# Performance work log

Hardware: AMD Instinct MI355X
Metric: run time of the kernel (lower is better)

Reference implementation:

```python
import jax, jax.numpy as jnp
import numpy as np

L = 2048  # episode_len
B = 64    # batch
K = 256   # key_size
V = 256   # value_size
H = 8     # num_head


def setup_inputs() -> dict:
    key = jax.random.key(0)
    ks = jax.random.split(key, 9)
    query = jax.random.normal(ks[0], (B, K), dtype=jnp.float32)
    keys = jax.random.normal(ks[1], (L, B, K), dtype=jnp.float32)
    vals = jax.random.normal(ks[2], (L, B, V), dtype=jnp.float32)
    rpe_mod = jax.random.uniform(ks[3], (L, B, 1), dtype=jnp.float32)
    Wq = jax.random.normal(ks[4], (K, H * K), dtype=jnp.float32) * (1.0 / np.sqrt(K))
    bq = jnp.zeros((H * K,), dtype=jnp.float32)
    Wa = jax.random.normal(ks[5], (H * V, V), dtype=jnp.float32) * (1.0 / np.sqrt(H * V))
    ba = jnp.zeros((V,), dtype=jnp.float32)
    # per-sample valid length in [1, L] (nonzero so the softmax is well-defined,
    # matching read()'s early-return guard for empty memories)
    steps = jax.random.randint(ks[6], (B,), 1, L + 1, dtype=jnp.int32)
    return {"query": query, "keys": keys, "vals": vals, "rpe_mod": rpe_mod,
            "Wq": Wq, "bq": bq, "Wa": Wa, "ba": ba, "steps": steps}


def reference(query, keys, vals, rpe_mod, Wq, bq, Wa, ba, steps):
    # query encoder: [B,K] -> [B,H,K]
    q = (query @ Wq + bq).reshape(B, H, K)
    # RPE-modulated keys: [L,B,K]
    mod_keys = keys * rpe_mod
    # scores[l,b,h] = <mod_keys[l,b,:], q[b,h,:]>
    scores = jnp.einsum('lbk,bhk->lbh', mod_keys, q)
    # mask out positions >= steps[b] (equivalent to slicing keys[:step[i], i])
    valid = (jnp.arange(L, dtype=jnp.int32)[:, None] < steps[None, :])  # [L,B]
    scores = jnp.where(valid[:, :, None], scores, -jnp.inf)
    weight = jax.nn.softmax(scores, axis=0)  # softmax over stored steps
    # weighted memory read: [B,H,V]
    read = jnp.einsum('lbh,lbv->bhv', weight, vals)
    # head aggregation: [B, H*V] -> [B, V]
    out = read.reshape(B, H * V) @ Wa + ba
    return out
```

## Files before the change

### kernel.cpp

```cpp
#include <hip/hip_runtime.h>
#include <hip/hip_bf16.h>
#include <cstdint>

#define Ln 2048
#define Bn 64
#define Kd 256
#define Vd 256
#define Hn 8

using u32 = unsigned int;
using u16 = unsigned short;

__device__ __forceinline__ float bflo(u32 u) { return __uint_as_float(u << 16); }
__device__ __forceinline__ float bfhi(u32 u) { return __uint_as_float(u & 0xffff0000u); }
__device__ __forceinline__ float bf1(u16 s) { return __uint_as_float(((u32)s) << 16); }

__device__ __forceinline__ bool sniff_bf16(const void* keys) {
  const u16* q = (const u16*)keys;
  int lane = threadIdx.x & 63;
  u16 u = q[2 * (lane * 127)];
  u32 e = (u >> 7) & 0xff;
  bool sane = (u == 0) || (e >= 100 && e <= 134);
  return __popcll(__ballot(sane)) > 32;
}

__global__ __launch_bounds__(256) void k_prep(const void* keys, const void* query,
                                              const void* Wq, const void* bq,
                                              float* q_ws) {
  const bool bf = sniff_bf16(keys);
  const int t = threadIdx.x;
  const int chunk = blockIdx.x;
  const int b = blockIdx.y;

  __shared__ float ql[256];
  ql[t] = bf ? bf1(((const u16*)query)[b * 256 + t]) : ((const float*)query)[b * 256 + t];
  __syncthreads();

  int c0 = chunk * 512 + 2 * t;
  float a0, a1;
  if (bf) { a0 = bf1(((const u16*)bq)[c0]); a1 = bf1(((const u16*)bq)[c0 + 1]); }
  else    { a0 = ((const float*)bq)[c0];    a1 = ((const float*)bq)[c0 + 1]; }

  if (bf) {
    const u32* w = (const u32*)Wq + chunk * 256 + t;
    for (int k0 = 0; k0 < 256; k0 += 16) {
      u32 wv[16];
#pragma unroll
      for (int j = 0; j < 16; j++) wv[j] = w[(size_t)(k0 + j) * 1024];
#pragma unroll
      for (int j = 0; j < 16; j++) {
        float qk = ql[k0 + j];
        a0 += qk * bflo(wv[j]); a1 += qk * bfhi(wv[j]);
      }
    }
  } else {
    const float2* w = (const float2*)Wq + chunk * 256 + t;
    for (int k0 = 0; k0 < 256; k0 += 16) {
      float2 wv[16];
#pragma unroll
      for (int j = 0; j < 16; j++) wv[j] = w[(size_t)(k0 + j) * 1024];
#pragma unroll
      for (int j = 0; j < 16; j++) {
        float qk = ql[k0 + j];
        a0 += qk * wv[j].x; a1 += qk * wv[j].y;
      }
    }
  }
  q_ws[b * 2048 + c0] = a0;
  q_ws[b * 2048 + c0 + 1] = a1;
}

__global__ __launch_bounds__(256) void k_fused(const void* keys, const void* vals,
                                               const void* rpe, const int* steps,
                                               const float* q_ws, float* O_part,
                                               float2* mz_part) {
  const int b = blockIdx.y, chunk = blockIdx.x;
  const int lstart = chunk * 128;
  const int stepb = steps[b];
  if (lstart >= stepb) return;
  const int lcnt_chunk = min(128, stepb - lstart);
  const bool bf = sniff_bf16(keys);
  const int t = threadIdx.x;
  const float* qb = q_ws + b * 2048;

  union Shm {
    struct { float ks[64 * 132]; float part[4][64][9]; } sc;
    float comb[128 * 20];
  };
  __shared__ Shm u;
  __shared__ __align__(16) float w_lds[128 * 12];
  __shared__ float rpe_lds[128];

  if (t < 128) {
    int l = lstart + t;
    rpe_lds[t] = bf ? bf1(((const u16*)rpe)[l * 64 + b]) : ((const float*)rpe)[l * 64 + b];
  }

  for (int st = 0; st < 2; st++) {
    const int sbase = st * 64;
    if (lstart + sbase >= stepb) continue;
    const int lcnt = min(64, stepb - lstart - sbase);
    const int r = t & 63;
    const int kh = __builtin_amdgcn_readfirstlane(t >> 6);
    float acc[8] = {0, 0, 0, 0, 0, 0, 0, 0};

    for (int khalf = 0; khalf < 2; khalf++) {
      __syncthreads();
      if (bf) {
        int r0 = t >> 4, c = t & 15;
#pragma unroll
        for (int rr = 0; rr < 4; rr++) {
          int row = r0 + rr * 16;
          const uint4* src = (const uint4*)((const u16*)keys +
              ((size_t)(lstart + sbase + row) * 64 + b) * 256 + khalf * 128);
          uint4 uu = src[c];
          float* dst = &u.sc.ks[row * 132 + c * 8];
          float4 lo, hi;
          lo.x = bflo(uu.x); lo.y = bfhi(uu.x); lo.z = bflo(uu.y); lo.w = bfhi(uu.y);
          hi.x = bflo(uu.z); hi.y = bfhi(uu.z); hi.z = bflo(uu.w); hi.w = bfhi(uu.w);
          *(float4*)dst = lo;
          *(float4*)(dst + 4) = hi;
        }
      } else {
        int r0 = t >> 5, c = t & 31;
#pragma unroll
        for (int rr = 0; rr < 8; rr++) {
          int row = r0 + rr * 8;
          const float4* src = (const float4*)((const float*)keys +
              ((size_t)(lstart + sbase + row) * 64 + b) * 256 + khalf * 128);
          *(float4*)&u.sc.ks[row * 132 + c * 4] = src[c];
        }
      }
      __syncthreads();
      if (r < lcnt) {
#pragma unroll
        for (int i = 0; i < 8; i++) {
          float4 kv = *(const float4*)&u.sc.ks[r * 132 + kh * 32 + 4 * i];
          int k0 = khalf * 128 + kh * 32 + 4 * i;
#pragma unroll
          for (int h = 0; h < 8; h++) {
            float4 qv = *(const float4*)&qb[h * 256 + k0];
            acc[h] += kv.x * qv.x + kv.y * qv.y + kv.z * qv.z + kv.w * qv.w;
          }
        }
      }
    }
    __syncthreads();
    if (r < lcnt) {
#pragma unroll
      for (int h = 0; h < 8; h++) u.sc.part[kh][r][h] = acc[h];
    }
    __syncthreads();
#pragma unroll
    for (int i = 0; i < 2; i++) {
      int idx = i * 256 + t;
      int h = idx >> 6, rr = idx & 63;
      if (rr < lcnt) {
        float s = u.sc.part[0][rr][h] + u.sc.part[1][rr][h] +
                  u.sc.part[2][rr][h] + u.sc.part[3][rr][h];
        w_lds[(sbase + rr) * 12 + h] = s * rpe_lds[sbase + rr];
      }
    }
  }
  __syncthreads();

  __shared__ float2 mz_lds[8];
  {
    const int h = t >> 5, j = t & 31;
    float m = -3.0e38f;
#pragma unroll
    for (int i = 0; i < 4; i++) {
      int l = j + 32 * i;
      if (l < lcnt_chunk) m = fmaxf(m, w_lds[l * 12 + h]);
    }
#pragma unroll
    for (int off = 16; off >= 1; off >>= 1) m = fmaxf(m, __shfl_xor(m, off, 32));
    float zs = 0.f;
#pragma unroll
    for (int i = 0; i < 4; i++) {
      int l = j + 32 * i;
      float e = 0.f;
      if (l < lcnt_chunk) e = __expf(w_lds[l * 12 + h] - m);
      w_lds[l * 12 + h] = e;
      zs += e;
    }
#pragma unroll
    for (int off = 16; off >= 1; off >>= 1) zs += __shfl_xor(zs, off, 32);
    if (j == 0) {
      float2 mz; mz.x = m; mz.y = zs;
      mz_lds[h] = mz;
    }
  }
  __syncthreads();
  if (t < 8) mz_part[((size_t)chunk * 64 + b) * 8 + t] = mz_lds[t];

  const int vp = t & 127;
  const int lh = __builtin_amdgcn_readfirstlane(t >> 7);
  float acc[8][2];
#pragma unroll
  for (int h = 0; h < 8; h++) { acc[h][0] = 0.f; acc[h][1] = 0.f; }

  if (bf) {
    const u32* vu = (const u32*)vals + ((size_t)(lstart + lh * 64) * 64 + b) * 128 + vp;
    for (int i0 = 0; i0 < 64; i0 += 8) {
      u32 uu[8];
#pragma unroll
      for (int j = 0; j < 8; j++) uu[j] = vu[(size_t)(i0 + j) * 8192];
#pragma unroll
      for (int j = 0; j < 8; j++) {
        int l = lh * 64 + i0 + j;
        float f0 = bflo(uu[j]), f1 = bfhi(uu[j]);
        float4 w0 = *(const float4*)&w_lds[l * 12];
        float4 w1 = *(const float4*)&w_lds[l * 12 + 4];
        acc[0][0] += w0.x * f0; acc[0][1] += w0.x * f1;
        acc[1][0] += w0.y * f0; acc[1][1] += w0.y * f1;
        acc[2][0] += w0.z * f0; acc[2][1] += w0.z * f1;
        acc[3][0] += w0.w * f0; acc[3][1] += w0.w * f1;
        acc[4][0] += w1.x * f0; acc[4][1] += w1.x * f1;
        acc[5][0] += w1.y * f0; acc[5][1] += w1.y * f1;
        acc[6][0] += w1.z * f0; acc[6][1] += w1.z * f1;
        acc[7][0] += w1.w * f0; acc[7][1] += w1.w * f1;
      }
    }
  } else {
    const float2* vf = (const float2*)vals + ((size_t)(lstart + lh * 64) * 64 + b) * 128 + vp;
    for (int i0 = 0; i0 < 64; i0 += 8) {
      float2 vv[8];
#pragma unroll
      for (int j = 0; j < 8; j++) vv[j] = vf[(size_t)(i0 + j) * 8192];
#pragma unroll
      for (int j = 0; j < 8; j++) {
        int l = lh * 64 + i0 + j;
        float4 w0 = *(const float4*)&w_lds[l * 12];
        float4 w1 = *(const float4*)&w_lds[l * 12 + 4];
        acc[0][0] += w0.x * vv[j].x; acc[0][1] += w0.x * vv[j].y;
        acc[1][0] += w0.y * vv[j].x; acc[1][1] += w0.y * vv[j].y;
        acc[2][0] += w0.z * vv[j].x; acc[2][1] += w0.z * vv[j].y;
        acc[3][0] += w0.w * vv[j].x; acc[3][1] += w0.w * vv[j].y;
        acc[4][0] += w1.x * vv[j].x; acc[4][1] += w1.x * vv[j].y;
        acc[5][0] += w1.y * vv[j].x; acc[5][1] += w1.y * vv[j].y;
        acc[6][0] += w1.z * vv[j].x; acc[6][1] += w1.z * vv[j].y;
        acc[7][0] += w1.w * vv[j].x; acc[7][1] += w1.w * vv[j].y;
      }
    }
  }
  __syncthreads();
  if (lh == 1) {
#pragma unroll
    for (int h = 0; h < 8; h++) {
      u.comb[vp * 20 + 2 * h] = acc[h][0];
      u.comb[vp * 20 + 2 * h + 1] = acc[h][1];
    }
  }
  __syncthreads();
  if (lh == 0) {
    float* op = O_part + ((size_t)chunk * 64 + b) * 2048;
#pragma unroll
    for (int h = 0; h < 8; h++) {
      float2 o;
      o.x = acc[h][0] + u.comb[vp * 20 + 2 * h];
      o.y = acc[h][1] + u.comb[vp * 20 + 2 * h + 1];
      *(float2*)&op[h * 256 + 2 * vp] = o;
    }
  }
}

__global__ __launch_bounds__(256) void k_out1(const void* keys, const void* Wa,
                                              const int* steps, const float* O_part,
                                              const float2* mz_part, float* out_part) {
  const int h = blockIdx.x, b = blockIdx.y;
  const bool bf = sniff_bf16(keys);
  const int t = threadIdx.x;
  const int nlive = (steps[b] + 127) >> 7;

  float2 mzv[16];
#pragma unroll
  for (int c = 0; c < 16; c++)
    mzv[c] = (c < nlive) ? mz_part[((size_t)c * 64 + b) * 8 + h] : make_float2(-3.0e38f, 0.f);
  float M = -3.0e38f;
#pragma unroll
  for (int c = 0; c < 16; c++) M = fmaxf(M, mzv[c].x);
  float sc[16];
  float Z = 0.f;
#pragma unroll
  for (int c = 0; c < 16; c++) {
    sc[c] = __expf(mzv[c].x - M);
    Z += sc[c] * mzv[c].y;
  }
  const float zi = 1.0f / Z;

  __shared__ float rn[256];
  {
    const float* op = O_part + (size_t)b * 2048 + h * 256 + t;
    float ov[16];
#pragma unroll
    for (int c = 0; c < 16; c++) ov[c] = (c < nlive) ? op[(size_t)c * 131072] : 0.f;
    float s = 0.f;
#pragma unroll
    for (int c = 0; c < 16; c++) s += sc[c] * ov[c];
    rn[t] = s * zi;
  }
  __syncthreads();

  float a = 0.f;
  if (bf) {
    const u32* wa = (const u32*)Wa + (size_t)(h * 256) * 128 + (t >> 1);
    const bool hi = (t & 1);
    for (int c0 = 0; c0 < 256; c0 += 16) {
      u32 wv[16];
#pragma unroll
      for (int j = 0; j < 16; j++) wv[j] = wa[(size_t)(c0 + j) * 128];
#pragma unroll
      for (int j = 0; j < 16; j++)
        a += rn[c0 + j] * (hi ? bfhi(wv[j]) : bflo(wv[j]));
    }
  } else {
    const float* wa = (const float*)Wa + (size_t)(h * 256) * 256 + t;
    for (int c0 = 0; c0 < 256; c0 += 16) {
      float wv[16];
#pragma unroll
      for (int j = 0; j < 16; j++) wv[j] = wa[(size_t)(c0 + j) * 256];
#pragma unroll
      for (int j = 0; j < 16; j++) a += rn[c0 + j] * wv[j];
    }
  }
  out_part[(size_t)(h * 64 + b) * 256 + t] = a;
}

__global__ __launch_bounds__(256) void k_out2(const void* keys, const void* ba,
                                              const float* out_part, void* out) {
  const int b = blockIdx.x, t = threadIdx.x;
  const bool bf = sniff_bf16(keys);
  float s = bf ? bf1(((const u16*)ba)[t]) : ((const float*)ba)[t];
  float ov[8];
#pragma unroll
  for (int h = 0; h < 8; h++) ov[h] = out_part[(size_t)(h * 64 + b) * 256 + t];
#pragma unroll
  for (int h = 0; h < 8; h++) s += ov[h];
  if (bf)
    ((__hip_bfloat16*)out)[b * 256 + t] = __float2bfloat16(s);
  else
    ((float*)out)[b * 256 + t] = s;
}

extern "C" void kernel_launch(void* const* d_in, const int* in_sizes, int n_in,
                              void* d_out, int out_size, void* d_ws, size_t ws_size,
                              hipStream_t stream) {
  (void)in_sizes; (void)n_in; (void)out_size; (void)ws_size;
  const void* query = d_in[0];
  const void* keys = d_in[1];
  const void* vals = d_in[2];
  const void* rpe = d_in[3];
  const void* Wq = d_in[4];
  const void* bq = d_in[5];
  const void* Wa = d_in[6];
  const void* ba = d_in[7];
  const int* steps = (const int*)d_in[8];

  float* ws = (float*)d_ws;
  float* q_ws = ws;
  float* O_part = ws + 131072;
  float2* mz_part = (float2*)(ws + 2228224);
  float* out_part = ws + 2244608;

  k_prep<<<dim3(4, 64), 256, 0, stream>>>(keys, query, Wq, bq, q_ws);
  k_fused<<<dim3(16, 64), 256, 0, stream>>>(keys, vals, rpe, steps, q_ws, O_part, mz_part);
  k_out1<<<dim3(8, 64), 256, 0, stream>>>(keys, Wa, steps, O_part, mz_part, out_part);
  k_out2<<<64, 256, 0, stream>>>(keys, ba, out_part, d_out);
}
```

Baseline: 318.1 us.

## Halve L-chunk size, keep query in registers, and software-pipeline key staging

Chunks along L shrink from 128 to 64 rows, doubling the grid to 32x64 blocks to raise parallelism and occupancy (launch bounds now ask for 4 blocks per SIMD). The score stage keeps each lane's query slice in registers and reduces with shuffles instead of reading q from global memory per row and combining partials in LDS. The second key half is loaded during compute on the first half. The value stage uses wider vector loads and reduces across lanes with shuffles instead of LDS. The cost is twice as many partial outputs for k_out1 to combine and a larger workspace.

```diff
diff --git a/kernel.cpp b/kernel.cpp
--- a/kernel.cpp
+++ b/kernel.cpp
@@ -7,6 +7,9 @@
 #define Kd 256
 #define Vd 256
 #define Hn 8
+
+#define CH 64
+#define NCH 32
 
 using u32 = unsigned int;
 using u16 = unsigned short;
@@ -70,197 +73,219 @@
   q_ws[b * 2048 + c0 + 1] = a1;
 }
 
-__global__ __launch_bounds__(256) void k_fused(const void* keys, const void* vals,
-                                               const void* rpe, const int* steps,
-                                               const float* q_ws, float* O_part,
-                                               float2* mz_part) {
+__global__ __launch_bounds__(256, 4) void k_fused(const void* keys, const void* vals,
+                                                  const void* rpe, const int* steps,
+                                                  const float* q_ws, float* O_part,
+                                                  float2* mz_part) {
   const int b = blockIdx.y, chunk = blockIdx.x;
-  const int lstart = chunk * 128;
+  const int lstart = chunk * CH;
   const int stepb = steps[b];
   if (lstart >= stepb) return;
-  const int lcnt_chunk = min(128, stepb - lstart);
+  const int lcnt = min(CH, stepb - lstart);
   const bool bf = sniff_bf16(keys);
   const int t = threadIdx.x;
-  const float* qb = q_ws + b * 2048;
-
-  union Shm {
-    struct { float ks[64 * 132]; float part[4][64][9]; } sc;
-    float comb[128 * 20];
-  };
-  __shared__ Shm u;
-  __shared__ __align__(16) float w_lds[128 * 12];
-  __shared__ float rpe_lds[128];
-
-  if (t < 128) {
+  const int lane = t & 63;
+  const int wave = __builtin_amdgcn_readfirstlane(t >> 6);
+
+  __shared__ __align__(16) float ks[CH * 132];
+  __shared__ __align__(16) float w_lds[CH * 12];
+  __shared__ float rpe_lds[CH];
+  __shared__ float2 mz_lds[8];
+
+  if (t < CH) {
     int l = lstart + t;
     rpe_lds[t] = bf ? bf1(((const u16*)rpe)[l * 64 + b]) : ((const float*)rpe)[l * 64 + b];
   }
 
-  for (int st = 0; st < 2; st++) {
-    const int sbase = st * 64;
-    if (lstart + sbase >= stepb) continue;
-    const int lcnt = min(64, stepb - lstart - sbase);
-    const int r = t & 63;
-    const int kh = __builtin_amdgcn_readfirstlane(t >> 6);
-    float acc[8] = {0, 0, 0, 0, 0, 0, 0, 0};
-
-    for (int khalf = 0; khalf < 2; khalf++) {
-      __syncthreads();
-      if (bf) {
-        int r0 = t >> 4, c = t & 15;
-#pragma unroll
-        for (int rr = 0; rr < 4; rr++) {
-          int row = r0 + rr * 16;
-          const uint4* src = (const uint4*)((const u16*)keys +
-              ((size_t)(lstart + sbase + row) * 64 + b) * 256 + khalf * 128);
-          uint4 uu = src[c];
-          float* dst = &u.sc.ks[row * 132 + c * 8];
-          float4 lo, hi;
-          lo.x = bflo(uu.x); lo.y = bfhi(uu.x); lo.z = bflo(uu.y); lo.w = bfhi(uu.y);
-          hi.x = bflo(uu.z); hi.y = bfhi(uu.z); hi.z = bflo(uu.w); hi.w = bfhi(uu.w);
-          *(float4*)dst = lo;
-          *(float4*)(dst + 4) = hi;
-        }
-      } else {
-        int r0 = t >> 5, c = t & 31;
-#pragma unroll
-        for (int rr = 0; rr < 8; rr++) {
-          int row = r0 + rr * 8;
-          const float4* src = (const float4*)((const float*)keys +
-              ((size_t)(lstart + sbase + row) * 64 + b) * 256 + khalf * 128);
-          *(float4*)&u.sc.ks[row * 132 + c * 4] = src[c];
-        }
-      }
-      __syncthreads();
-      if (r < lcnt) {
-#pragma unroll
-        for (int i = 0; i < 8; i++) {
-          float4 kv = *(const float4*)&u.sc.ks[r * 132 + kh * 32 + 4 * i];
-          int k0 = khalf * 128 + kh * 32 + 4 * i;
-#pragma unroll
-          for (int h = 0; h < 8; h++) {
-            float4 qv = *(const float4*)&qb[h * 256 + k0];
-            acc[h] += kv.x * qv.x + kv.y * qv.y + kv.z * qv.z + kv.w * qv.w;
-          }
-        }
-      }
-    }
-    __syncthreads();
-    if (r < lcnt) {
-#pragma unroll
-      for (int h = 0; h < 8; h++) u.sc.part[kh][r][h] = acc[h];
-    }
-    __syncthreads();
-#pragma unroll
-    for (int i = 0; i < 2; i++) {
-      int idx = i * 256 + t;
-      int h = idx >> 6, rr = idx & 63;
-      if (rr < lcnt) {
-        float s = u.sc.part[0][rr][h] + u.sc.part[1][rr][h] +
-                  u.sc.part[2][rr][h] + u.sc.part[3][rr][h];
-        w_lds[(sbase + rr) * 12 + h] = s * rpe_lds[sbase + rr];
-      }
+  const int h8 = lane >> 3, ks8 = lane & 7;
+  float4 qreg[8];
+  {
+    const float* qb = q_ws + b * 2048 + h8 * 256 + ks8 * 4;
+#pragma unroll
+    for (int j = 0; j < 8; j++) qreg[j] = *(const float4*)&qb[j * 32];
+  }
+
+  float accs[16];
+#pragma unroll
+  for (int r = 0; r < 16; r++) accs[r] = 0.f;
+
+  auto COMPUTE = [&](int kh2) {
+    const int rowbase = wave * 16;
+    const float4 q0 = qreg[kh2 * 4 + 0], q1 = qreg[kh2 * 4 + 1];
+    const float4 q2 = qreg[kh2 * 4 + 2], q3 = qreg[kh2 * 4 + 3];
+#pragma unroll
+    for (int r = 0; r < 16; r++) {
+      const float* kp = &ks[(rowbase + r) * 132 + ks8 * 4];
+      float4 k0 = *(const float4*)kp;
+      float4 k1 = *(const float4*)(kp + 32);
+      float4 k2 = *(const float4*)(kp + 64);
+      float4 k3 = *(const float4*)(kp + 96);
+      float a = accs[r];
+      a += k0.x * q0.x + k0.y * q0.y + k0.z * q0.z + k0.w * q0.w;
+      a += k1.x * q1.x + k1.y * q1.y + k1.z * q1.z + k1.w * q1.w;
+      a += k2.x * q2.x + k2.y * q2.y + k2.z * q2.z + k2.w * q2.w;
+      a += k3.x * q3.x + k3.y * q3.y + k3.z * q3.z + k3.w * q3.w;
+      accs[r] = a;
+    }
+  };
+
+  if (bf) {
+    const int c = t & 15, r0 = t >> 4;
+    auto LOADB = [&](int kh2, uint4* uu) {
+      const u16* srcb = (const u16*)keys + ((size_t)(lstart + r0) * 64 + b) * 256 + kh2 * 128;
+#pragma unroll
+      for (int rr = 0; rr < 4; rr++)
+        uu[rr] = *((const uint4*)(srcb + (size_t)rr * 16 * 16384) + c);
+    };
+    auto WRITEB = [&](const uint4* uu) {
+#pragma unroll
+      for (int rr = 0; rr < 4; rr++) {
+        int row = r0 + rr * 16;
+        float* dst = &ks[row * 132 + c * 8];
+        float4 lo, hi;
+        lo.x = bflo(uu[rr].x); lo.y = bfhi(uu[rr].x); lo.z = bflo(uu[rr].y); lo.w = bfhi(uu[rr].y);
+        hi.x = bflo(uu[rr].z); hi.y = bfhi(uu[rr].z); hi.z = bflo(uu[rr].w); hi.w = bfhi(uu[rr].w);
+        *(float4*)dst = lo;
+        *(float4*)(dst + 4) = hi;
+      }
+    };
+    uint4 su[4];
+    LOADB(0, su); WRITEB(su);
+    __syncthreads();
+    LOADB(1, su);
+    COMPUTE(0);
+    __syncthreads();
+    WRITEB(su);
+    __syncthreads();
+    COMPUTE(1);
+  } else {
+    const int c = t & 31, r0 = t >> 5;
+    auto LOADF = [&](int kh2, float4* vv) {
+      const float* src = (const float*)keys + ((size_t)(lstart + r0) * 64 + b) * 256 + kh2 * 128 + c * 4;
+#pragma unroll
+      for (int rr = 0; rr < 8; rr++) vv[rr] = *(const float4*)(src + (size_t)rr * 8 * 16384);
+    };
+    auto WRITEF = [&](const float4* vv) {
+#pragma unroll
+      for (int rr = 0; rr < 8; rr++) *(float4*)&ks[(r0 + rr * 8) * 132 + c * 4] = vv[rr];
+    };
+    float4 sv[8];
+    LOADF(0, sv); WRITEF(sv);
+    __syncthreads();
+    LOADF(1, sv);
+    COMPUTE(0);
+    __syncthreads();
+    WRITEF(sv);
+    __syncthreads();
+    COMPUTE(1);
+  }
+
+  {
+    const int rowbase = wave * 16;
+#pragma unroll
+    for (int r = 0; r < 16; r++) {
+      float v = accs[r];
+      v += __shfl_xor(v, 1);
+      v += __shfl_xor(v, 2);
+      v += __shfl_xor(v, 4);
+      if (ks8 == 0) w_lds[(rowbase + r) * 12 + h8] = v * rpe_lds[rowbase + r];
     }
   }
   __syncthreads();
 
-  __shared__ float2 mz_lds[8];
   {
     const int h = t >> 5, j = t & 31;
-    float m = -3.0e38f;
-#pragma unroll
-    for (int i = 0; i < 4; i++) {
-      int l = j + 32 * i;
-      if (l < lcnt_chunk) m = fmaxf(m, w_lds[l * 12 + h]);
-    }
+    float s0 = (j < lcnt) ? w_lds[j * 12 + h] : -3.0e38f;
+    float s1 = (j + 32 < lcnt) ? w_lds[(j + 32) * 12 + h] : -3.0e38f;
+    float m = fmaxf(s0, s1);
 #pragma unroll
     for (int off = 16; off >= 1; off >>= 1) m = fmaxf(m, __shfl_xor(m, off, 32));
-    float zs = 0.f;
-#pragma unroll
-    for (int i = 0; i < 4; i++) {
-      int l = j + 32 * i;
-      float e = 0.f;
-      if (l < lcnt_chunk) e = __expf(w_lds[l * 12 + h] - m);
-      w_lds[l * 12 + h] = e;
-      zs += e;
-    }
+    float e0 = (j < lcnt) ? __expf(s0 - m) : 0.f;
+    float e1 = (j + 32 < lcnt) ? __expf(s1 - m) : 0.f;
+    w_lds[j * 12 + h] = e0;
+    w_lds[(j + 32) * 12 + h] = e1;
+    float zs = e0 + e1;
 #pragma unroll
     for (int off = 16; off >= 1; off >>= 1) zs += __shfl_xor(zs, off, 32);
-    if (j == 0) {
-      float2 mz; mz.x = m; mz.y = zs;
-      mz_lds[h] = mz;
-    }
+    if (j == 0) mz_lds[h] = make_float2(m, zs);
   }
   __syncthreads();
   if (t < 8) mz_part[((size_t)chunk * 64 + b) * 8 + t] = mz_lds[t];
 
-  const int vp = t & 127;
-  const int lh = __builtin_amdgcn_readfirstlane(t >> 7);
-  float acc[8][2];
-#pragma unroll
-  for (int h = 0; h < 8; h++) { acc[h][0] = 0.f; acc[h][1] = 0.f; }
+  const int vslot = lane & 15, rg = lane >> 4;
+  float acc[8][4];
+#pragma unroll
+  for (int hh = 0; hh < 8; hh++)
+#pragma unroll
+    for (int cc = 0; cc < 4; cc++) acc[hh][cc] = 0.f;
 
   if (bf) {
-    const u32* vu = (const u32*)vals + ((size_t)(lstart + lh * 64) * 64 + b) * 128 + vp;
-    for (int i0 = 0; i0 < 64; i0 += 8) {
-      u32 uu[8];
-#pragma unroll
-      for (int j = 0; j < 8; j++) uu[j] = vu[(size_t)(i0 + j) * 8192];
-#pragma unroll
-      for (int j = 0; j < 8; j++) {
-        int l = lh * 64 + i0 + j;
-        float f0 = bflo(uu[j]), f1 = bfhi(uu[j]);
-        float4 w0 = *(const float4*)&w_lds[l * 12];
-        float4 w1 = *(const float4*)&w_lds[l * 12 + 4];
-        acc[0][0] += w0.x * f0; acc[0][1] += w0.x * f1;
-        acc[1][0] += w0.y * f0; acc[1][1] += w0.y * f1;
-        acc[2][0] += w0.z * f0; acc[2][1] += w0.z * f1;
-        acc[3][0] += w0.w * f0; acc[3][1] += w0.w * f1;
-        acc[4][0] += w1.x * f0; acc[4][1] += w1.x * f1;
-        acc[5][0] += w1.y * f0; acc[5][1] += w1.y * f1;
-        acc[6][0] += w1.z * f0; acc[6][1] += w1.z * f1;
-        acc[7][0] += w1.w * f0; acc[7][1] += w1.w * f1;
+    const u32* vb = (const u32*)vals + ((size_t)lstart * 64 + b) * 128 + wave * 32 + vslot * 2;
+    for (int i0 = 0; i0 < 16; i0 += 8) {
+      uint2 uu[8];
+#pragma unroll
+      for (int jb = 0; jb < 8; jb++) {
+        int row = rg + 4 * (i0 + jb);
+        uu[jb] = *(const uint2*)(vb + (size_t)row * 8192);
+      }
+#pragma unroll
+      for (int jb = 0; jb < 8; jb++) {
+        int row = rg + 4 * (i0 + jb);
+        float4 w0 = *(const float4*)&w_lds[row * 12];
+        float4 w1 = *(const float4*)&w_lds[row * 12 + 4];
+        float v0 = bflo(uu[jb].x), v1 = bfhi(uu[jb].x);
+        float v2 = bflo(uu[jb].y), v3 = bfhi(uu[jb].y);
+        acc[0][0] += w0.x * v0; acc[0][1] += w0.x * v1; acc[0][2] += w0.x * v2; acc[0][3] += w0.x * v3;
+        acc[1][0] += w0.y * v0; acc[1][1] += w0.y * v1; acc[1][2] += w0.y * v2; acc[1][3] += w0.y * v3;
+        acc[2][0] += w0.z * v0; acc[2][1] += w0.z * v1; acc[2][2] += w0.z * v2; acc[2][3] += w0.z * v3;
+        acc[3][0] += w0.w * v0; acc[3][1] += w0.w * v1; acc[3][2] += w0.w * v2; acc[3][3] += w0.w * v3;
+        acc[4][0] += w1.x * v0; acc[4][1] += w1.x * v1; acc[4][2] += w1.x * v2; acc[4][3] += w1.x * v3;
+        acc[5][0] += w1.y * v0; acc[5][1] += w1.y * v1; acc[5][2] += w1.y * v2; acc[5][3] += w1.y * v3;
+        acc[6][0] += w1.z * v0; acc[6][1] += w1.z * v1; acc[6][2] += w1.z * v2; acc[6][3] += w1.z * v3;
+        acc[7][0] += w1.w * v0; acc[7][1] += w1.w * v1; acc[7][2] += w1.w * v2; acc[7][3] += w1.w * v3;
       }
     }
   } else {
-    const float2* vf = (const float2*)vals + ((size_t)(lstart + lh * 64) * 64 + b) * 128 + vp;
-    for (int i0 = 0; i0 < 64; i0 += 8) {
-      float2 vv[8];
-#pragma unroll
-      for (int j = 0; j < 8; j++) vv[j] = vf[(size_t)(i0 + j) * 8192];
-#pragma unroll
-      for (int j = 0; j < 8; j++) {
-        int l = lh * 64 + i0 + j;
-        float4 w0 = *(const float4*)&w_lds[l * 12];
-        float4 w1 = *(const float4*)&w_lds[l * 12 + 4];
-        acc[0][0] += w0.x * vv[j].x; acc[0][1] += w0.x * vv[j].y;
-        acc[1][0] += w0.y * vv[j].x; acc[1][1] += w0.y * vv[j].y;
-        acc[2][0] += w0.z * vv[j].x; acc[2][1] += w0.z * vv[j].y;
-        acc[3][0] += w0.w * vv[j].x; acc[3][1] += w0.w * vv[j].y;
-        acc[4][0] += w1.x * vv[j].x; acc[4][1] += w1.x * vv[j].y;
-        acc[5][0] += w1.y * vv[j].x; acc[5][1] += w1.y * vv[j].y;
-        acc[6][0] += w1.z * vv[j].x; acc[6][1] += w1.z * vv[j].y;
-        acc[7][0] += w1.w * vv[j].x; acc[7][1] += w1.w * vv[j].y;
-      }
-    }
-  }
-  __syncthreads();
-  if (lh == 1) {
-#pragma unroll
-    for (int h = 0; h < 8; h++) {
-      u.comb[vp * 20 + 2 * h] = acc[h][0];
-      u.comb[vp * 20 + 2 * h + 1] = acc[h][1];
-    }
-  }
-  __syncthreads();
-  if (lh == 0) {
-    float* op = O_part + ((size_t)chunk * 64 + b) * 2048;
-#pragma unroll
-    for (int h = 0; h < 8; h++) {
-      float2 o;
-      o.x = acc[h][0] + u.comb[vp * 20 + 2 * h];
-      o.y = acc[h][1] + u.comb[vp * 20 + 2 * h + 1];
-      *(float2*)&op[h * 256 + 2 * vp] = o;
+    const float* vb = (const float*)vals + ((size_t)lstart * 64 + b) * 256 + wave * 64 + vslot * 4;
+    for (int i0 = 0; i0 < 16; i0 += 8) {
+      float4 vv[8];
+#pragma unroll
+      for (int jb = 0; jb < 8; jb++) {
+        int row = rg + 4 * (i0 + jb);
+        vv[jb] = *(const float4*)(vb + (size_t)row * 16384);
+      }
+#pragma unroll
+      for (int jb = 0; jb < 8; jb++) {
+        int row = rg + 4 * (i0 + jb);
+        float4 w0 = *(const float4*)&w_lds[row * 12];
+        float4 w1 = *(const float4*)&w_lds[row * 12 + 4];
+        acc[0][0] += w0.x * vv[jb].x; acc[0][1] += w0.x * vv[jb].y; acc[0][2] += w0.x * vv[jb].z; acc[0][3] += w0.x * vv[jb].w;
+        acc[1][0] += w0.y * vv[jb].x; acc[1][1] += w0.y * vv[jb].y; acc[1][2] += w0.y * vv[jb].z; acc[1][3] += w0.y * vv[jb].w;
+        acc[2][0] += w0.z * vv[jb].x; acc[2][1] += w0.z * vv[jb].y; acc[2][2] += w0.z * vv[jb].z; acc[2][3] += w0.z * vv[jb].w;
+        acc[3][0] += w0.w * vv[jb].x; acc[3][1] += w0.w * vv[jb].y; acc[3][2] += w0.w * vv[jb].z; acc[3][3] += w0.w * vv[jb].w;
+        acc[4][0] += w1.x * vv[jb].x; acc[4][1] += w1.x * vv[jb].y; acc[4][2] += w1.x * vv[jb].z; acc[4][3] += w1.x * vv[jb].w;
+        acc[5][0] += w1.y * vv[jb].x; acc[5][1] += w1.y * vv[jb].y; acc[5][2] += w1.y * vv[jb].z; acc[5][3] += w1.y * vv[jb].w;
+        acc[6][0] += w1.z * vv[jb].x; acc[6][1] += w1.z * vv[jb].y; acc[6][2] += w1.z * vv[jb].z; acc[6][3] += w1.z * vv[jb].w;
+        acc[7][0] += w1.w * vv[jb].x; acc[7][1] += w1.w * vv[jb].y; acc[7][2] += w1.w * vv[jb].z; acc[7][3] += w1.w * vv[jb].w;
+      }
+    }
+  }
+
+#pragma unroll
+  for (int hh = 0; hh < 8; hh++)
+#pragma unroll
+    for (int cc = 0; cc < 4; cc++) {
+      float v = acc[hh][cc];
+      v += __shfl_xor(v, 16);
+      v += __shfl_xor(v, 32);
+      acc[hh][cc] = v;
+    }
+  if (rg == 0) {
+    float* op = O_part + ((size_t)chunk * 64 + b) * 2048 + wave * 64 + vslot * 4;
+#pragma unroll
+    for (int hh = 0; hh < 8; hh++) {
+      float4 o = make_float4(acc[hh][0], acc[hh][1], acc[hh][2], acc[hh][3]);
+      *(float4*)&op[hh * 256] = o;
     }
   }
 }
@@ -271,19 +296,19 @@
   const int h = blockIdx.x, b = blockIdx.y;
   const bool bf = sniff_bf16(keys);
   const int t = threadIdx.x;
-  const int nlive = (steps[b] + 127) >> 7;
-
-  float2 mzv[16];
-#pragma unroll
-  for (int c = 0; c < 16; c++)
+  const int nlive = (steps[b] + CH - 1) >> 6;
+
+  float2 mzv[NCH];
+#pragma unroll
+  for (int c = 0; c < NCH; c++)
     mzv[c] = (c < nlive) ? mz_part[((size_t)c * 64 + b) * 8 + h] : make_float2(-3.0e38f, 0.f);
   float M = -3.0e38f;
 #pragma unroll
-  for (int c = 0; c < 16; c++) M = fmaxf(M, mzv[c].x);
-  float sc[16];
+  for (int c = 0; c < NCH; c++) M = fmaxf(M, mzv[c].x);
+  float sc[NCH];
   float Z = 0.f;
 #pragma unroll
-  for (int c = 0; c < 16; c++) {
+  for (int c = 0; c < NCH; c++) {
     sc[c] = __expf(mzv[c].x - M);
     Z += sc[c] * mzv[c].y;
   }
@@ -292,12 +317,16 @@
   __shared__ float rn[256];
   {
     const float* op = O_part + (size_t)b * 2048 + h * 256 + t;
+    float s = 0.f;
     float ov[16];
 #pragma unroll
     for (int c = 0; c < 16; c++) ov[c] = (c < nlive) ? op[(size_t)c * 131072] : 0.f;
-    float s = 0.f;
 #pragma unroll
     for (int c = 0; c < 16; c++) s += sc[c] * ov[c];
+#pragma unroll
+    for (int c = 0; c < 16; c++) ov[c] = (c + 16 < nlive) ? op[(size_t)(c + 16) * 131072] : 0.f;
+#pragma unroll
+    for (int c = 0; c < 16; c++) s += sc[c + 16] * ov[c];
     rn[t] = s * zi;
   }
   __syncthreads();
@@ -360,11 +389,11 @@
   float* ws = (float*)d_ws;
   float* q_ws = ws;
   float* O_part = ws + 131072;
-  float2* mz_part = (float2*)(ws + 2228224);
-  float* out_part = ws + 2244608;
+  float2* mz_part = (float2*)(ws + 131072 + 4194304);
+  float* out_part = ws + 131072 + 4194304 + 32768;
 
   k_prep<<<dim3(4, 64), 256, 0, stream>>>(keys, query, Wq, bq, q_ws);
-  k_fused<<<dim3(16, 64), 256, 0, stream>>>(keys, vals, rpe, steps, q_ws, O_part, mz_part);
+  k_fused<<<dim3(NCH, 64), 256, 0, stream>>>(keys, vals, rpe, steps, q_ws, O_part, mz_part);
   k_out1<<<dim3(8, 64), 256, 0, stream>>>(keys, Wa, steps, O_part, mz_part, out_part);
   k_out2<<<64, 256, 0, stream>>>(keys, ba, out_part, d_out);
 }
```

Result: slower. 327.6 us (+3.0%).
